# Kernel tuning notes

Hardware: AMD Instinct MI355X
Metric: run time of the kernel (lower is better)

## Reference

```python
import jax, jax.numpy as jnp
import numpy as np

B, T, C, FFN, N_LAYER, LAYER_ID = 4, 2048, 1024, 4096, 24, 1
EPS = 1e-5


def setup_inputs() -> dict:
    key = jax.random.key(0)
    ks = jax.random.split(key, 10)
    scale = 0.02

    def w(k, shape):
        return (jax.random.normal(k, shape, jnp.float32) * scale)

    # RWKV-4 init formulas for layer_id=1, n_layer=24 (learned params, init per source)
    r01 = LAYER_ID / (N_LAYER - 1)
    r10 = 1.0 - LAYER_ID / N_LAYER
    ddd = np.arange(C, dtype=np.float64) / C
    h = np.arange(C, dtype=np.float64)
    decay = -5.0 + 8.0 * (h / (C - 1)) ** (0.7 + 1.3 * r01)
    zigzag = np.array([(i + 1) % 3 - 1 for i in range(C)], dtype=np.float64) * 0.5
    tfirst = np.log(0.3) + zigzag

    return {
        "x": jax.random.normal(ks[0], (B, T, C), jnp.float32),
        "ln1_w": jnp.ones((C,), jnp.float32), "ln1_b": jnp.zeros((C,), jnp.float32),
        "ln2_w": jnp.ones((C,), jnp.float32), "ln2_b": jnp.zeros((C,), jnp.float32),
        "time_decay": jnp.asarray(decay, jnp.float32),
        "time_first": jnp.asarray(tfirst, jnp.float32),
        "tmk": jnp.asarray(ddd ** r10, jnp.float32),
        "tmv": jnp.asarray(ddd ** r10 + 0.3 * r01, jnp.float32),
        "tmr": jnp.asarray(ddd ** (0.5 * r10), jnp.float32),
        "att_kw": w(ks[1], (C, C)), "att_vw": w(ks[2], (C, C)),
        "att_rw": w(ks[3], (C, C)), "att_ow": w(ks[4], (C, C)),
        "f_tmk": jnp.asarray(ddd ** r10, jnp.float32),
        "f_tmr": jnp.asarray(ddd ** r10, jnp.float32),
        "f_kw": w(ks[5], (FFN, C)), "f_rw": w(ks[6], (C, C)), "f_vw": w(ks[7], (C, FFN)),
    }


def _ln(z, g, b):
    m = jnp.mean(z, axis=-1, keepdims=True)
    v = jnp.mean(jnp.square(z - m), axis=-1, keepdims=True)
    return (z - m) * jax.lax.rsqrt(v + EPS) * g + b


def _shift(z):  # token shift: prepend zero row along T, drop last
    return jnp.pad(z, ((0, 0), (1, 0), (0, 0)))[:, :-1]


def _wkv(time_decay, u, k, v):
    # Numerically-stable RWKV-4 WKV recurrence (log-space max trick).
    # k, v: [B, T, C]; time_decay, u: [C]
    w = -jnp.exp(time_decay)  # per-channel decay (negative)
    kt = jnp.moveaxis(k, 1, 0)  # [T, B, C]
    vt = jnp.moveaxis(v, 1, 0)
    aa = jnp.zeros_like(kt[0])
    bb = jnp.zeros_like(kt[0])
    pp = jnp.full_like(kt[0], -1e38)

    def step(carry, kv):
        aa, bb, pp = carry
        kk, vv = kv
        ww = u + kk
        p = jnp.maximum(pp, ww)
        e1 = jnp.exp(pp - p)
        e2 = jnp.exp(ww - p)
        out = (e1 * aa + e2 * vv) / (e1 * bb + e2)
        ww2 = pp + w
        p2 = jnp.maximum(ww2, kk)
        e1b = jnp.exp(ww2 - p2)
        e2b = jnp.exp(kk - p2)
        return (e1b * aa + e2b * vv, e1b * bb + e2b, p2), out

    _, out = jax.lax.scan(step, (aa, bb, pp), (kt, vt))
    return jnp.moveaxis(out, 0, 1)  # [B, T, C]


def reference(x, ln1_w, ln1_b, ln2_w, ln2_b, time_decay, time_first,
              tmk, tmv, tmr, att_kw, att_vw, att_rw, att_ow,
              f_tmk, f_tmr, f_kw, f_rw, f_vw):
    # --- RWKV_TimeMix (layer_id != 0; protectors are identity in fwd for finite vals) ---
    h = _ln(x, ln1_w, ln1_b)
    hx = _shift(h)
    xk = h * tmk + hx * (1.0 - tmk)
    xv = h * tmv + hx * (1.0 - tmv)
    xr = h * tmr + hx * (1.0 - tmr)
    k = jnp.einsum('btc,dc->btd', xk, att_kw)
    v = jnp.einsum('btc,dc->btd', xv, att_vw)
    sr = jax.nn.sigmoid(jnp.einsum('btc,dc->btd', xr, att_rw))
    rwkv = sr * _wkv(time_decay, time_first, k, v)
    x = x + jnp.einsum('btd,cd->btc', rwkv, att_ow)
    # --- RWKV_ChannelMix ---
    h = _ln(x, ln2_w, ln2_b)
    hx = _shift(h)
    xk = h * f_tmk + hx * (1.0 - f_tmk)
    xr = h * f_tmr + hx * (1.0 - f_tmr)
    kk = jnp.square(jax.nn.relu(jnp.einsum('btc,fc->btf', xk, f_kw)))
    kv = jnp.einsum('btf,cf->btc', kk, f_vw)
    x = x + jax.nn.sigmoid(jnp.einsum('btc,dc->btd', xr, f_rw)) * kv
    return x
```

## Files before the change

### kernel.cpp

```cpp
#include <hip/hip_runtime.h>
#include <cstdint>

#define C_DIM 1024
#define T_DIM 2048
#define B_DIM 4
#define FFN_DIM 4096
#define NROWS (B_DIM * T_DIM)
#define NELEM ((size_t)NROWS * C_DIM)
#define MB ((size_t)1 << 20)
#define NSEG 32
#define SEGL (T_DIM / NSEG)

typedef __bf16 bf16;
typedef __bf16 bf16x4 __attribute__((ext_vector_type(4)));
typedef __bf16 bf16x8 __attribute__((ext_vector_type(8)));
typedef float  floatx4 __attribute__((ext_vector_type(4)));

#define GLDS(g, l) __builtin_amdgcn_global_load_lds(                          \
    (const __attribute__((address_space(1))) void*)(g),                       \
    (__attribute__((address_space(3))) void*)(l), 16, 0, 0)

struct W7 {
    const float* s[7];
    bf16*        d[7];
    int          cum[8];
};

__global__ __launch_bounds__(256) void f2b7_kernel(W7 w)
{
    int id = blockIdx.x * 256 + threadIdx.x;
    int seg = 0;
#pragma unroll
    for (int j = 1; j < 7; ++j) if (id >= w.cum[j]) seg = j;
    int i = id - w.cum[seg];
    float4 v = ((const float4*)w.s[seg])[i];
    bf16x4 o = { (bf16)v.x, (bf16)v.y, (bf16)v.z, (bf16)v.w };
    ((bf16x4*)w.d[seg])[i] = o;
}

template<bool HASV>
__global__ __launch_bounds__(256) void lnmix_kernel(const float* __restrict__ x,
                                                    const float* __restrict__ g,
                                                    const float* __restrict__ b,
                                                    const float* __restrict__ mk,
                                                    const float* __restrict__ mv,
                                                    const float* __restrict__ mr,
                                                    bf16* __restrict__ xk,
                                                    bf16* __restrict__ xv,
                                                    bf16* __restrict__ xr)
{
    int row = blockIdx.x;
    int t   = row & (T_DIM - 1);
    int tid = threadIdx.x;
    size_t i4 = (size_t)row * 256 + tid;

    float4 v  = ((const float4*)x)[i4];
    float4 vp = make_float4(0.f, 0.f, 0.f, 0.f);
    if (t != 0) vp = ((const float4*)x)[i4 - 256];

    float s   = v.x + v.y + v.z + v.w;
    float s2  = v.x * v.x + v.y * v.y + v.z * v.z + v.w * v.w;
    float sp  = vp.x + vp.y + vp.z + vp.w;
    float sp2 = vp.x * vp.x + vp.y * vp.y + vp.z * vp.z + vp.w * vp.w;
    for (int off = 32; off > 0; off >>= 1) {
        s   += __shfl_down(s,   off);
        s2  += __shfl_down(s2,  off);
        sp  += __shfl_down(sp,  off);
        sp2 += __shfl_down(sp2, off);
    }
    __shared__ float red[16];
    int lane = tid & 63, wid = tid >> 6;
    if (lane == 0) { red[wid] = s; red[4 + wid] = s2; red[8 + wid] = sp; red[12 + wid] = sp2; }
    __syncthreads();
    s   = red[0] + red[1] + red[2] + red[3];
    s2  = red[4] + red[5] + red[6] + red[7];
    sp  = red[8] + red[9] + red[10] + red[11];
    sp2 = red[12] + red[13] + red[14] + red[15];

    float mean  = s * (1.0f / C_DIM);
    float inv   = rsqrtf(s2 * (1.0f / C_DIM) - mean * mean + 1e-5f);
    float meanp = sp * (1.0f / C_DIM);
    float invp  = rsqrtf(sp2 * (1.0f / C_DIM) - meanp * meanp + 1e-5f);

    float4 gv = ((const float4*)g)[tid];
    float4 bv = ((const float4*)b)[tid];
    float4 hv, hp;
    hv.x = (v.x - mean) * inv * gv.x + bv.x;
    hv.y = (v.y - mean) * inv * gv.y + bv.y;
    hv.z = (v.z - mean) * inv * gv.z + bv.z;
    hv.w = (v.w - mean) * inv * gv.w + bv.w;
    if (t != 0) {
        hp.x = (vp.x - meanp) * invp * gv.x + bv.x;
        hp.y = (vp.y - meanp) * invp * gv.y + bv.y;
        hp.z = (vp.z - meanp) * invp * gv.z + bv.z;
        hp.w = (vp.w - meanp) * invp * gv.w + bv.w;
    } else {
        hp = make_float4(0.f, 0.f, 0.f, 0.f);
    }

    float4 m1 = ((const float4*)mk)[tid];
    bf16x4 o;
    o.x = (bf16)(hp.x + m1.x * (hv.x - hp.x));
    o.y = (bf16)(hp.y + m1.y * (hv.y - hp.y));
    o.z = (bf16)(hp.z + m1.z * (hv.z - hp.z));
    o.w = (bf16)(hp.w + m1.w * (hv.w - hp.w));
    ((bf16x4*)xk)[i4] = o;

    if (HASV) {
        float4 m2 = ((const float4*)mv)[tid];
        o.x = (bf16)(hp.x + m2.x * (hv.x - hp.x));
        o.y = (bf16)(hp.y + m2.y * (hv.y - hp.y));
        o.z = (bf16)(hp.z + m2.z * (hv.z - hp.z));
        o.w = (bf16)(hp.w + m2.w * (hv.w - hp.w));
        ((bf16x4*)xv)[i4] = o;
    }

    float4 m3 = ((const float4*)mr)[tid];
    o.x = (bf16)(hp.x + m3.x * (hv.x - hp.x));
    o.y = (bf16)(hp.y + m3.y * (hv.y - hp.y));
    o.z = (bf16)(hp.z + m3.z * (hv.z - hp.z));
    o.w = (bf16)(hp.w + m3.w * (hv.w - hp.w));
    ((bf16x4*)xr)[i4] = o;
}

#define EPI_NONE 0
#define EPI_SIG 1
#define EPI_RELU2 2
#define EPI_ADD 3
#define EPI_SCALEADD 4

struct GemmProb {
    const bf16* A;
    const bf16* W;
    void*       Y;
    const float* X2;
    const bf16*  S;
    int N, K, epi, outBf16;
};
struct GemmBatch {
    GemmProb p[3];
    int cum[4];
};

template<int BN>
__global__ __launch_bounds__(256) void gemm_bat(GemmBatch bat)
{
    constexpr int NJ   = BN / 32;
    constexpr int ABUF = 128 * 32;
    constexpr int BBUF = BN * 32;
    __shared__ unsigned short As[2 * ABUF];
    __shared__ unsigned short Bs[2 * BBUF];

    int tid = threadIdx.x;
    int id  = blockIdx.x;
    int pi  = (id >= bat.cum[1]) + (id >= bat.cum[2]);
    const bf16* PA = bat.p[pi].A;
    const bf16* PW = bat.p[pi].W;
    void*       PY = bat.p[pi].Y;
    const float* PX2 = bat.p[pi].X2;
    const bf16*  PS  = bat.p[pi].S;
    int N = bat.p[pi].N, K = bat.p[pi].K;
    int epi = bat.p[pi].epi, obf = bat.p[pi].outBf16;
    int lid = id - bat.cum[pi];

    int ntn    = N / BN;
    int stride = ntn >> 3;
    int sh     = __ffs(stride) - 1;
    int sq  = lid >> 3;
    int n_t = (lid & 7) * stride + (sq & (stride - 1));
    int m_t = sq >> sh;
    int m0 = m_t * 128, n0 = n_t * BN;

    int r0  = tid >> 2;
    int qsw = ((tid & 3) - ((r0 >> 1) & 3)) & 3;
    const bf16* Ag = PA + (size_t)(m0 + r0) * K + qsw * 8;
    const bf16* Wg = PW + (size_t)(n0 + r0) * K + qsw * 8;
    size_t rowK = (size_t)64 * K;
    int wv = tid >> 6;
    unsigned short* AsW0 = As + wv * 512;
    unsigned short* AsW1 = As + 2048 + wv * 512;
    unsigned short* BsW0 = Bs + wv * 512;
    unsigned short* BsW1 = Bs + (BN == 128 ? 2048 : 0) + wv * 512;

    int ln = tid & 63;
    int wm = (wv & 1) * 64, wn = (wv >> 1) * (BN / 2);
    int ra0 = wm + (ln & 15);
    int rb0 = wn + (ln & 15);
    int qa  = ln >> 4;
    int abase = ra0 * 32 + (((qa + (ra0 >> 1)) & 3) * 8);
    int bbase = rb0 * 32 + (((qa + (rb0 >> 1)) & 3) * 8);

    floatx4 acc[4][NJ] = {};

#define STAGE_TILE(kt, bi)                                                    \
    do {                                                                      \
        int _ko = (kt) << 5;                                                  \
        GLDS(Ag + _ko,        AsW0 + (bi) * ABUF);                            \
        GLDS(Ag + _ko + rowK, AsW1 + (bi) * ABUF);                            \
        GLDS(Wg + _ko,        BsW0 + (bi) * BBUF);                            \
        if constexpr (BN == 128) GLDS(Wg + _ko + rowK, BsW1 + (bi) * BBUF);   \
    } while (0)

#define CONSUME(bi)                                                           \
    do {                                                                      \
        const unsigned short* Ac = As + (bi) * ABUF + abase;                  \
        const unsigned short* Bc = Bs + (bi) * BBUF + bbase;                  \
        bf16x8 a[4], b[NJ];                                                   \
        _Pragma("unroll")                                                     \
        for (int i = 0; i < 4; ++i) a[i] = *(const bf16x8*)(Ac + i * 512);    \
        _Pragma("unroll")                                                     \
        for (int j = 0; j < NJ; ++j) b[j] = *(const bf16x8*)(Bc + j * 512);   \
        asm volatile("s_waitcnt lgkmcnt(0)" ::: "memory");                    \
        __builtin_amdgcn_sched_barrier(0);                       \
        _Pragma("unroll")                                                     \
        for (int i = 0; i < 4; ++i)                                           \
            _Pragma("unroll")                                                 \
            for (int j = 0; j < NJ; ++j)                                      \
                acc[i][j] = __builtin_amdgcn_mfma_f32_16x16x32_bf16(          \
                    a[i], b[j], acc[i][j], 0, 0, 0);                          \
    } while (0)

    int nt = K >> 5;

    STAGE_TILE(0, 0);
    STAGE_TILE(1, 1);

    int cur = 0;
    for (int t = 0; t < nt - 1; ++t) {
        if constexpr (BN == 128) asm volatile("s_waitcnt vmcnt(4)" ::: "memory");
        else                     asm volatile("s_waitcnt vmcnt(3)" ::: "memory");
        __builtin_amdgcn_s_barrier();
        __builtin_amdgcn_sched_barrier(0);
        CONSUME(cur);
        __builtin_amdgcn_s_barrier();
        if (t + 2 < nt) STAGE_TILE(t + 2, cur);
        cur ^= 1;
    }
    asm volatile("s_waitcnt vmcnt(0)" ::: "memory");
    __builtin_amdgcn_s_barrier();
    __builtin_amdgcn_sched_barrier(0);
    CONSUME(cur);

#undef STAGE_TILE
#undef CONSUME

    int row0 = (ln >> 4) * 4;
    int colb = n0 + wn + (ln & 15);
#pragma unroll
    for (int i = 0; i < 4; ++i) {
        int gm = m0 + wm + i * 16 + row0;
#pragma unroll
        for (int j = 0; j < NJ; ++j) {
            int gn = colb + j * 16;
#pragma unroll
            for (int r = 0; r < 4; ++r) {
                size_t idx = (size_t)(gm + r) * N + gn;
                float v = acc[i][j][r];
                if (epi == EPI_SIG)        v = 1.0f / (1.0f + __expf(-v));
                else if (epi == EPI_RELU2) { float t2 = fmaxf(v, 0.0f); v = t2 * t2; }
                else if (epi == EPI_ADD)   v = PX2[idx] + v;
                else if (epi == EPI_SCALEADD) v = PX2[idx] + (float)PS[idx] * v;
                if (obf) ((bf16*)PY)[idx] = (bf16)v;
                else     ((float*)PY)[idx] = v;
            }
        }
    }
}

__global__ __launch_bounds__(256) void wkv_seg(const float* __restrict__ k,
                                               const float* __restrict__ v,
                                               const float* __restrict__ decay,
                                               float* __restrict__ sa,
                                               float* __restrict__ sb,
                                               float* __restrict__ sp)
{
    int idx = blockIdx.x * 256 + threadIdx.x;
    int c   = idx & (C_DIM - 1);
    int bs  = idx >> 10;
    int seg = bs & (NSEG - 1);
    int b   = bs >> 5;
    float w = -__expf(decay[c]);
    size_t base = ((size_t)b * T_DIM + (size_t)seg * SEGL) * C_DIM + c;
    float aa = 0.f, bb = 0.f, pp = -1e38f;
    for (int t = 0; t < SEGL; ++t) {
        size_t off = base + (size_t)t * C_DIM;
        float kk = k[off], vv = v[off];
        float ww2 = pp + w;
        float p2  = fmaxf(ww2, kk);
        float e1  = __expf(ww2 - p2);
        float e2  = __expf(kk - p2);
        aa = e1 * aa + e2 * vv;
        bb = e1 * bb + e2;
        pp = p2;
    }
    sa[idx] = aa; sb[idx] = bb; sp[idx] = pp;
}

__global__ __launch_bounds__(256) void wkv_comb(const float* __restrict__ sa,
                                                const float* __restrict__ sb,
                                                const float* __restrict__ sp,
                                                const float* __restrict__ decay,
                                                float* __restrict__ ia,
                                                float* __restrict__ ib,
                                                float* __restrict__ ip)
{
    int idx = blockIdx.x * 256 + threadIdx.x;
    int c = idx & (C_DIM - 1);
    int b = idx >> 10;
    float wL = -__expf(decay[c]) * (float)SEGL;
    float aa = 0.f, bb = 0.f, pp = -1e38f;
    size_t base = (size_t)b * NSEG * C_DIM + c;
    for (int j = 0; j < NSEG; ++j) {
        size_t o = base + (size_t)j * C_DIM;
        ia[o] = aa; ib[o] = bb; ip[o] = pp;
        float a_s = sa[o], b_s = sb[o], p_s = sp[o];
        float pd = pp + wL;
        float pn = fmaxf(pd, p_s);
        float e1 = __expf(pd - pn);
        float e2 = __expf(p_s - pn);
        aa = e1 * aa + e2 * a_s;
        bb = e1 * bb + e2 * b_s;
        pp = pn;
    }
}

__global__ __launch_bounds__(256) void wkv_out(const float* __restrict__ k,
                                               const float* __restrict__ v,
                                               const bf16* __restrict__ sr,
                                               const float* __restrict__ decay,
                                               const float* __restrict__ first,
                                               const float* __restrict__ ia,
                                               const float* __restrict__ ib,
                                               const float* __restrict__ ip,
                                               bf16* __restrict__ out)
{
    int idx = blockIdx.x * 256 + threadIdx.x;
    int c   = idx & (C_DIM - 1);
    int bs  = idx >> 10;
    int seg = bs & (NSEG - 1);
    int b   = bs >> 5;
    float w = -__expf(decay[c]);
    float u = first[c];
    float aa = ia[idx], bb = ib[idx], pp = ip[idx];
    size_t base = ((size_t)b * T_DIM + (size_t)seg * SEGL) * C_DIM + c;
    for (int t = 0; t < SEGL; ++t) {
        size_t off = base + (size_t)t * C_DIM;
        float kk = k[off], vv = v[off];
        float ww = u + kk;
        float p  = fmaxf(pp, ww);
        float e1 = __expf(pp - p);
        float e2 = __expf(ww - p);
        float o  = (e1 * aa + e2 * vv) / (e1 * bb + e2);
        out[off] = (bf16)((float)sr[off] * o);
        float ww2 = pp + w;
        float p2  = fmaxf(ww2, kk);
        float e1b = __expf(ww2 - p2);
        float e2b = __expf(kk - p2);
        aa = e1b * aa + e2b * vv;
        bb = e1b * bb + e2b;
        pp = p2;
    }
}

extern "C" void kernel_launch(void* const* d_in, const int* in_sizes, int n_in,
                              void* d_out, int out_size, void* d_ws, size_t ws_size,
                              hipStream_t stream)
{
    const float* x          = (const float*)d_in[0];
    const float* ln1_w      = (const float*)d_in[1];
    const float* ln1_b      = (const float*)d_in[2];
    const float* ln2_w      = (const float*)d_in[3];
    const float* ln2_b      = (const float*)d_in[4];
    const float* time_decay = (const float*)d_in[5];
    const float* time_first = (const float*)d_in[6];
    const float* tmk        = (const float*)d_in[7];
    const float* tmv        = (const float*)d_in[8];
    const float* tmr        = (const float*)d_in[9];
    const float* att_kw     = (const float*)d_in[10];
    const float* att_vw     = (const float*)d_in[11];
    const float* att_rw     = (const float*)d_in[12];
    const float* att_ow     = (const float*)d_in[13];
    const float* f_tmk      = (const float*)d_in[14];
    const float* f_tmr      = (const float*)d_in[15];
    const float* f_kw       = (const float*)d_in[16];
    const float* f_rw       = (const float*)d_in[17];
    const float* f_vw       = (const float*)d_in[18];
    float* out = (float*)d_out;

    char* W8 = (char*)d_ws;
    bf16* kw_b  = (bf16*)(W8 + 0 * MB);
    bf16* vw_b  = (bf16*)(W8 + 2 * MB);
    bf16* rw_b  = (bf16*)(W8 + 4 * MB);
    bf16* ow_b  = (bf16*)(W8 + 6 * MB);
    bf16* fkw_b = (bf16*)(W8 + 8 * MB);
    bf16* frw_b = (bf16*)(W8 + 16 * MB);
    bf16* fvw_b = (bf16*)(W8 + 18 * MB);

    bf16*  xk_b   = (bf16*)(W8 + 26 * MB);
    bf16*  xv_b   = (bf16*)(W8 + 42 * MB);
    bf16*  xr_b   = (bf16*)(W8 + 58 * MB);
    bf16*  rwkv_b = xk_b;
    bf16*  xk2_b  = (bf16*)(W8 + 26 * MB);
    bf16*  xr2_b  = (bf16*)(W8 + 42 * MB);
    bf16*  sr2_b  = (bf16*)(W8 + 58 * MB);
    float* kbuf   = (float*)(W8 + 74 * MB);
    float* vbuf   = (float*)(W8 + 106 * MB);
    bf16*  srb_b  = (bf16*)(W8 + 138 * MB);
    bf16*  kk_b   = (bf16*)(W8 + 106 * MB);

    size_t KB512 = (size_t)512 * 1024;
    float* sc_a = (float*)(W8 + 170 * MB);
    float* sc_b = (float*)(W8 + 170 * MB + 1 * KB512);
    float* sc_p = (float*)(W8 + 170 * MB + 2 * KB512);
    float* in_a = (float*)(W8 + 170 * MB + 3 * KB512);
    float* in_b = (float*)(W8 + 170 * MB + 4 * KB512);
    float* in_p = (float*)(W8 + 170 * MB + 5 * KB512);

    int nC4 = C_DIM * C_DIM / 4, nF4 = FFN_DIM * C_DIM / 4;
    W7 w7;
    const float* srcs[7] = { att_kw, att_vw, att_rw, att_ow, f_kw, f_rw, f_vw };
    bf16*        dsts[7] = { kw_b, vw_b, rw_b, ow_b, fkw_b, frw_b, fvw_b };
    int          cnts[7] = { nC4, nC4, nC4, nC4, nF4, nC4, nF4 };
    int cum = 0;
    for (int i = 0; i < 7; ++i) { w7.s[i] = srcs[i]; w7.d[i] = dsts[i]; w7.cum[i] = cum; cum += cnts[i]; }
    w7.cum[7] = cum;
    f2b7_kernel<<<cum / 256, 256, 0, stream>>>(w7);

    int segGrid = B_DIM * NSEG * C_DIM / 256;

    auto prob = [](const bf16* A, const bf16* W, void* Y, const float* X2,
                   const bf16* S, int N, int K, int epi, int obf) {
        GemmProb p; p.A = A; p.W = W; p.Y = Y; p.X2 = X2; p.S = S;
        p.N = N; p.K = K; p.epi = epi; p.outBf16 = obf; return p;
    };

    lnmix_kernel<true><<<NROWS, 256, 0, stream>>>(x, ln1_w, ln1_b, tmk, tmv, tmr,
                                                  xk_b, xv_b, xr_b);
    {
        GemmBatch b3;
        b3.p[0] = prob(xk_b, kw_b, kbuf,  nullptr, nullptr, C_DIM, C_DIM, EPI_NONE, 0);
        b3.p[1] = prob(xv_b, vw_b, vbuf,  nullptr, nullptr, C_DIM, C_DIM, EPI_NONE, 0);
        b3.p[2] = prob(xr_b, rw_b, srb_b, nullptr, nullptr, C_DIM, C_DIM, EPI_SIG,  1);
        b3.cum[0] = 0; b3.cum[1] = 512; b3.cum[2] = 1024; b3.cum[3] = 1536;
        gemm_bat<128><<<1536, 256, 0, stream>>>(b3);
    }
    wkv_seg<<<segGrid, 256, 0, stream>>>(kbuf, vbuf, time_decay, sc_a, sc_b, sc_p);
    wkv_comb<<<B_DIM * C_DIM / 256, 256, 0, stream>>>(sc_a, sc_b, sc_p, time_decay, in_a, in_b, in_p);
    wkv_out<<<segGrid, 256, 0, stream>>>(kbuf, vbuf, srb_b, time_decay, time_first,
                                         in_a, in_b, in_p, rwkv_b);
    {
        GemmBatch b1;
        b1.p[0] = prob(rwkv_b, ow_b, out, x, nullptr, C_DIM, C_DIM, EPI_ADD, 0);
        b1.p[1] = b1.p[0]; b1.p[2] = b1.p[0];
        b1.cum[0] = 0; b1.cum[1] = 1024; b1.cum[2] = 1024; b1.cum[3] = 1024;
        gemm_bat<64><<<1024, 256, 0, stream>>>(b1);
    }

    lnmix_kernel<false><<<NROWS, 256, 0, stream>>>(out, ln2_w, ln2_b, f_tmk, nullptr, f_tmr,
                                                   xk2_b, nullptr, xr2_b);
    {
        GemmBatch b2;
        b2.p[0] = prob(xk2_b, fkw_b, kk_b,  nullptr, nullptr, FFN_DIM, C_DIM, EPI_RELU2, 1);
        b2.p[1] = prob(xr2_b, frw_b, sr2_b, nullptr, nullptr, C_DIM,   C_DIM, EPI_SIG,   1);
        b2.p[2] = b2.p[1];
        b2.cum[0] = 0; b2.cum[1] = 2048; b2.cum[2] = 2560; b2.cum[3] = 2560;
        gemm_bat<128><<<2560, 256, 0, stream>>>(b2);
    }
    {
        GemmBatch b1;
        b1.p[0] = prob(kk_b, fvw_b, out, out, sr2_b, C_DIM, FFN_DIM, EPI_SCALEADD, 0);
        b1.p[1] = b1.p[0]; b1.p[2] = b1.p[0];
        b1.cum[0] = 0; b1.cum[1] = 1024; b1.cum[2] = 1024; b1.cum[3] = 1024;
        gemm_bat<64><<<1024, 256, 0, stream>>>(b1);
    }
}
```

Before: 578.9 us.

## Replace batched multi-problem GEMM launches with separate fixed 128x128 GEMM kernels

Removes the GemmBatch multi-problem dispatch and the BN=64 template variant, launching one single-problem 128x128-tile GEMM kernel per matrix product. This drops the per-block problem selection and simplifies the kernel. The trade-off is more kernel launches, and fewer blocks for the N=1024 output GEMMs, which may leave compute units underused.

After: 592.8 us. 2.4% more time.

```diff
diff --git a/kernel.cpp b/kernel.cpp
--- a/kernel.cpp
+++ b/kernel.cpp
@@ -129,7 +129,7 @@
 #define EPI_ADD 3
 #define EPI_SCALEADD 4
 
-struct GemmProb {
+struct GemmArgs {
     const bf16* A;
     const bf16* W;
     void*       Y;
@@ -137,39 +137,31 @@
     const bf16*  S;
     int N, K, epi, outBf16;
 };
-struct GemmBatch {
-    GemmProb p[3];
-    int cum[4];
-};
-
-template<int BN>
-__global__ __launch_bounds__(256) void gemm_bat(GemmBatch bat)
-{
-    constexpr int NJ   = BN / 32;
+
+__global__ __launch_bounds__(256) void gemm_p(GemmArgs pr)
+{
     constexpr int ABUF = 128 * 32;
-    constexpr int BBUF = BN * 32;
+    constexpr int BBUF = 128 * 32;
     __shared__ unsigned short As[2 * ABUF];
     __shared__ unsigned short Bs[2 * BBUF];
 
     int tid = threadIdx.x;
-    int id  = blockIdx.x;
-    int pi  = (id >= bat.cum[1]) + (id >= bat.cum[2]);
-    const bf16* PA = bat.p[pi].A;
-    const bf16* PW = bat.p[pi].W;
-    void*       PY = bat.p[pi].Y;
-    const float* PX2 = bat.p[pi].X2;
-    const bf16*  PS  = bat.p[pi].S;
-    int N = bat.p[pi].N, K = bat.p[pi].K;
-    int epi = bat.p[pi].epi, obf = bat.p[pi].outBf16;
-    int lid = id - bat.cum[pi];
-
-    int ntn    = N / BN;
+    int lid = blockIdx.x;
+    const bf16* PA = pr.A;
+    const bf16* PW = pr.W;
+    void*       PY = pr.Y;
+    const float* PX2 = pr.X2;
+    const bf16*  PS  = pr.S;
+    int N = pr.N, K = pr.K;
+    int epi = pr.epi, obf = pr.outBf16;
+
+    int ntn    = N >> 7;
     int stride = ntn >> 3;
     int sh     = __ffs(stride) - 1;
     int sq  = lid >> 3;
     int n_t = (lid & 7) * stride + (sq & (stride - 1));
     int m_t = sq >> sh;
-    int m0 = m_t * 128, n0 = n_t * BN;
+    int m0 = m_t * 128, n0 = n_t * 128;
 
     int r0  = tid >> 2;
     int qsw = ((tid & 3) - ((r0 >> 1) & 3)) & 3;
@@ -180,17 +172,17 @@
     unsigned short* AsW0 = As + wv * 512;
     unsigned short* AsW1 = As + 2048 + wv * 512;
     unsigned short* BsW0 = Bs + wv * 512;
-    unsigned short* BsW1 = Bs + (BN == 128 ? 2048 : 0) + wv * 512;
+    unsigned short* BsW1 = Bs + 2048 + wv * 512;
 
     int ln = tid & 63;
-    int wm = (wv & 1) * 64, wn = (wv >> 1) * (BN / 2);
+    int wm = (wv & 1) * 64, wn = (wv >> 1) * 64;
     int ra0 = wm + (ln & 15);
     int rb0 = wn + (ln & 15);
     int qa  = ln >> 4;
     int abase = ra0 * 32 + (((qa + (ra0 >> 1)) & 3) * 8);
     int bbase = rb0 * 32 + (((qa + (rb0 >> 1)) & 3) * 8);
 
-    floatx4 acc[4][NJ] = {};
+    floatx4 acc[4][4] = {};
 
 #define STAGE_TILE(kt, bi)                                                    \
     do {                                                                      \
@@ -198,24 +190,24 @@
         GLDS(Ag + _ko,        AsW0 + (bi) * ABUF);                            \
         GLDS(Ag + _ko + rowK, AsW1 + (bi) * ABUF);                            \
         GLDS(Wg + _ko,        BsW0 + (bi) * BBUF);                            \
-        if constexpr (BN == 128) GLDS(Wg + _ko + rowK, BsW1 + (bi) * BBUF);   \
+        GLDS(Wg + _ko + rowK, BsW1 + (bi) * BBUF);                            \
     } while (0)
 
 #define CONSUME(bi)                                                           \
     do {                                                                      \
         const unsigned short* Ac = As + (bi) * ABUF + abase;                  \
         const unsigned short* Bc = Bs + (bi) * BBUF + bbase;                  \
-        bf16x8 a[4], b[NJ];                                                   \
+        bf16x8 a[4], b[4];                                                    \
         _Pragma("unroll")                                                     \
         for (int i = 0; i < 4; ++i) a[i] = *(const bf16x8*)(Ac + i * 512);    \
         _Pragma("unroll")                                                     \
-        for (int j = 0; j < NJ; ++j) b[j] = *(const bf16x8*)(Bc + j * 512);   \
+        for (int j = 0; j < 4; ++j) b[j] = *(const bf16x8*)(Bc + j * 512);    \
         asm volatile("s_waitcnt lgkmcnt(0)" ::: "memory");                    \
         __builtin_amdgcn_sched_barrier(0);                       \
         _Pragma("unroll")                                                     \
         for (int i = 0; i < 4; ++i)                                           \
             _Pragma("unroll")                                                 \
-            for (int j = 0; j < NJ; ++j)                                      \
+            for (int j = 0; j < 4; ++j)                                       \
                 acc[i][j] = __builtin_amdgcn_mfma_f32_16x16x32_bf16(          \
                     a[i], b[j], acc[i][j], 0, 0, 0);                          \
     } while (0)
@@ -227,8 +219,7 @@
 
     int cur = 0;
     for (int t = 0; t < nt - 1; ++t) {
-        if constexpr (BN == 128) asm volatile("s_waitcnt vmcnt(4)" ::: "memory");
-        else                     asm volatile("s_waitcnt vmcnt(3)" ::: "memory");
+        asm volatile("s_waitcnt vmcnt(4)" ::: "memory");
         __builtin_amdgcn_s_barrier();
         __builtin_amdgcn_sched_barrier(0);
         CONSUME(cur);
@@ -250,7 +241,7 @@
     for (int i = 0; i < 4; ++i) {
         int gm = m0 + wm + i * 16 + row0;
 #pragma unroll
-        for (int j = 0; j < NJ; ++j) {
+        for (int j = 0; j < 4; ++j) {
             int gn = colb + j * 16;
 #pragma unroll
             for (int r = 0; r < 4; ++r) {
@@ -428,49 +419,28 @@
 
     int segGrid = B_DIM * NSEG * C_DIM / 256;
 
-    auto prob = [](const bf16* A, const bf16* W, void* Y, const float* X2,
-                   const bf16* S, int N, int K, int epi, int obf) {
-        GemmProb p; p.A = A; p.W = W; p.Y = Y; p.X2 = X2; p.S = S;
-        p.N = N; p.K = K; p.epi = epi; p.outBf16 = obf; return p;
+    auto launch = [&](const bf16* A, const bf16* W, void* Y, const float* X2,
+                      const bf16* S, int N, int K, int epi, int obf) {
+        GemmArgs p; p.A = A; p.W = W; p.Y = Y; p.X2 = X2; p.S = S;
+        p.N = N; p.K = K; p.epi = epi; p.outBf16 = obf;
+        int grid = (NROWS / 128) * (N / 128);
+        gemm_p<<<grid, 256, 0, stream>>>(p);
     };
 
     lnmix_kernel<true><<<NROWS, 256, 0, stream>>>(x, ln1_w, ln1_b, tmk, tmv, tmr,
                                                   xk_b, xv_b, xr_b);
-    {
-        GemmBatch b3;
-        b3.p[0] = prob(xk_b, kw_b, kbuf,  nullptr, nullptr, C_DIM, C_DIM, EPI_NONE, 0);
-        b3.p[1] = prob(xv_b, vw_b, vbuf,  nullptr, nullptr, C_DIM, C_DIM, EPI_NONE, 0);
-        b3.p[2] = prob(xr_b, rw_b, srb_b, nullptr, nullptr, C_DIM, C_DIM, EPI_SIG,  1);
-        b3.cum[0] = 0; b3.cum[1] = 512; b3.cum[2] = 1024; b3.cum[3] = 1536;
-        gemm_bat<128><<<1536, 256, 0, stream>>>(b3);
-    }
+    launch(xk_b, kw_b, kbuf,  nullptr, nullptr, C_DIM, C_DIM, EPI_NONE, 0);
+    launch(xv_b, vw_b, vbuf,  nullptr, nullptr, C_DIM, C_DIM, EPI_NONE, 0);
+    launch(xr_b, rw_b, srb_b, nullptr, nullptr, C_DIM, C_DIM, EPI_SIG,  1);
     wkv_seg<<<segGrid, 256, 0, stream>>>(kbuf, vbuf, time_decay, sc_a, sc_b, sc_p);
     wkv_comb<<<B_DIM * C_DIM / 256, 256, 0, stream>>>(sc_a, sc_b, sc_p, time_decay, in_a, in_b, in_p);
     wkv_out<<<segGrid, 256, 0, stream>>>(kbuf, vbuf, srb_b, time_decay, time_first,
                                          in_a, in_b, in_p, rwkv_b);
-    {
-        GemmBatch b1;
-        b1.p[0] = prob(rwkv_b, ow_b, out, x, nullptr, C_DIM, C_DIM, EPI_ADD, 0);
-        b1.p[1] = b1.p[0]; b1.p[2] = b1.p[0];
-        b1.cum[0] = 0; b1.cum[1] = 1024; b1.cum[2] = 1024; b1.cum[3] = 1024;
-        gemm_bat<64><<<1024, 256, 0, stream>>>(b1);
-    }
+    launch(rwkv_b, ow_b, out, x, nullptr, C_DIM, C_DIM, EPI_ADD, 0);
 
     lnmix_kernel<false><<<NROWS, 256, 0, stream>>>(out, ln2_w, ln2_b, f_tmk, nullptr, f_tmr,
                                                    xk2_b, nullptr, xr2_b);
-    {
-        GemmBatch b2;
-        b2.p[0] = prob(xk2_b, fkw_b, kk_b,  nullptr, nullptr, FFN_DIM, C_DIM, EPI_RELU2, 1);
-        b2.p[1] = prob(xr2_b, frw_b, sr2_b, nullptr, nullptr, C_DIM,   C_DIM, EPI_SIG,   1);
-        b2.p[2] = b2.p[1];
-        b2.cum[0] = 0; b2.cum[1] = 2048; b2.cum[2] = 2560; b2.cum[3] = 2560;
-        gemm_bat<128><<<2560, 256, 0, stream>>>(b2);
-    }
-    {
-        GemmBatch b1;
-        b1.p[0] = prob(kk_b, fvw_b, out, out, sr2_b, C_DIM, FFN_DIM, EPI_SCALEADD, 0);
-        b1.p[1] = b1.p[0]; b1.p[2] = b1.p[0];
-        b1.cum[0] = 0; b1.cum[1] = 1024; b1.cum[2] = 1024; b1.cum[3] = 1024;
-        gemm_bat<64><<<1024, 256, 0, stream>>>(b1);
-    }
-}
+    launch(xr2_b, frw_b, sr2_b, nullptr, nullptr, C_DIM,   C_DIM, EPI_SIG,   1);
+    launch(xk2_b, fkw_b, kk_b,  nullptr, nullptr, FFN_DIM, C_DIM, EPI_RELU2, 1);
+    launch(kk_b,  fvw_b, out,   out,     sr2_b,   C_DIM, FFN_DIM, EPI_SCALEADD, 0);
+}
```
